# Performance work log

Hardware: AMD Instinct MI355X
Metric: run time of the kernel (lower is better)

The kernel has to match this reference:

```python
import jax, jax.numpy as jnp
import numpy as np

B, T, N, M = 128, 128, 32, 128  # batch, window(input_len), driving_series, hidden_size


def _lstm_cell(x_t, h, c, Wih, Whh, bih, bhh):
    # PyTorch gate order: i, f, g, o
    g = x_t @ Wih.T + bih + h @ Whh.T + bhh
    i, f, gg, o = jnp.split(g, 4, axis=-1)
    c = jax.nn.sigmoid(f) * c + jax.nn.sigmoid(i) * jnp.tanh(gg)
    h = jax.nn.sigmoid(o) * jnp.tanh(c)
    return h, c


def _lstm_seq(x, Wih, Whh, bih, bhh):
    # x: [B,T,n] -> outputs [B,T,m], zero init state
    Bc = x.shape[0]
    m = Whh.shape[1]
    def step(carry, x_t):
        h, c = carry
        h, c = _lstm_cell(x_t, h, c, Wih, Whh, bih, bhh)
        return (h, c), h
    h0 = jnp.zeros((Bc, m), x.dtype)
    (_, _), ys = jax.lax.scan(step, (h0, h0), jnp.swapaxes(x, 0, 1))
    return jnp.swapaxes(ys, 0, 1)


def _forward(x, Wih0, Whh0, bih0, bhh0, We, Ue, Ve,
             Wg, bg, Wa, ba,
             Wih1, Whh1, bih1, bhh1, Wih2, Whh2, bih2, bhh2):
    Bc, Tc, n = x.shape
    m = Whh0.shape[1]
    ux = jnp.einsum('btn,mn->btm', x, Ue)  # Ue(x), constant across steps

    def step(carry, x_t):
        h, c = carry
        hs = jnp.concatenate([h, c], axis=-1)              # [B,2m]
        e = jnp.tanh(ux + (hs @ We.T)[:, None, :]) @ Ve[0]  # [B,T]
        a = jax.nn.softmax(e, axis=1)
        ia_t = jnp.einsum('bt,btn->bn', a, x)              # attended input at step t
        h, c = _lstm_cell(x_t, h, c, Wih0, Whh0, bih0, bhh0)
        return (h, c), ia_t

    h0 = jnp.zeros((Bc, m), x.dtype)
    (_, _), ia = jax.lax.scan(step, (h0, h0), jnp.swapaxes(x, 0, 1))
    input_attention = jnp.swapaxes(ia, 0, 1)               # [B,T,n]

    # self (spatial) attention, fully vectorized over t
    g = jnp.tanh(jnp.einsum('btn,mn->btm', x, Wg) + bg)
    a = jax.nn.sigmoid(jnp.einsum('btm,nm->btn', g, Wa) + ba)
    self_attention = a * x                                  # [B,T,n]

    out1 = _lstm_seq(input_attention, Wih1, Whh1, bih1, bhh1)
    out2 = _lstm_seq(self_attention, Wih2, Whh2, bih2, bhh2)
    return jnp.concatenate([out1, out2], axis=-1)           # [B,T,2m]


def setup_inputs() -> dict:
    key = jax.random.key(0)
    ks = jax.random.split(key, 20)
    stdv = 1.0 / np.sqrt(M)
    u = lambda k, shp: jax.random.uniform(k, shp, jnp.float32, -stdv, stdv)
    inp = {
        'x': jax.random.normal(ks[0], (B, T, N), jnp.float32),
        'Wih0': u(ks[1], (4 * M, N)), 'Whh0': u(ks[2], (4 * M, M)),
        'bih0': u(ks[3], (4 * M,)), 'bhh0': u(ks[4], (4 * M,)),
        'We': u(ks[5], (M, 2 * M)), 'Ue': u(ks[6], (M, N)), 'Ve': u(ks[7], (1, M)),
        'Wg': u(ks[8], (M, N)), 'bg': u(ks[9], (M,)),
        'Wa': u(ks[10], (N, M)), 'ba': u(ks[11], (N,)),
        'Wih1': u(ks[12], (4 * M, N)), 'Whh1': u(ks[13], (4 * M, M)),
        'bih1': u(ks[14], (4 * M,)), 'bhh1': u(ks[15], (4 * M,)),
        'Wih2': u(ks[16], (4 * M, N)), 'Whh2': u(ks[17], (4 * M, M)),
        'bih2': u(ks[18], (4 * M,)), 'bhh2': u(ks[19], (4 * M,)),
    }
    return inp


def reference(x, Wih0, Whh0, bih0, bhh0, We, Ue, Ve, Wg, bg, Wa, ba,
              Wih1, Whh1, bih1, bhh1, Wih2, Whh2, bih2, bhh2):
    return _forward(x, Wih0, Whh0, bih0, bhh0, We, Ue, Ve, Wg, bg, Wa, ba,
                    Wih1, Whh1, bih1, bhh1, Wih2, Whh2, bih2, bhh2)
```

## Files before the change

### kernel.cpp

```cpp
#include <hip/hip_runtime.h>

#define DI __device__ __forceinline__

DI float frcp(float v)  { return __builtin_amdgcn_rcpf(v); }
DI float fsig(float v)  { return frcp(1.0f + __expf(-v)); }
DI float ftanh(float v) { return 1.0f - 2.0f * frcp(__expf(2.0f * v) + 1.0f); }
DI float dot4(float4 a, float4 b) { return a.x*b.x + a.y*b.y + a.z*b.z + a.w*b.w; }

DI unsigned bf16r(float f) {
    unsigned b = __float_as_uint(f);
    return (b + 0x7fffu + ((b >> 16) & 1u)) >> 16;
}
DI unsigned bfpack(float f0, float f1) { return bf16r(f0) | (bf16r(f1) << 16); }
DI float blo(unsigned u) { return __uint_as_float(u << 16); }
DI float bhi(unsigned u) { return __uint_as_float(u & 0xffff0000u); }

template <int MODE>
DI void lstm_scan3(const float* __restrict__ xin,
                   const float* __restrict__ Wih,
                   const float* __restrict__ Whh,
                   const float* __restrict__ bih,
                   const float* __restrict__ bhh,
                   float* __restrict__ rec,
                   float* __restrict__ outp,
                   float* lds)
{
    const int tid = threadIdx.x;
    const int r0 = tid & 127;
    const int kq = tid >> 7;
    float* xl = lds;
    float* hl = lds + 4096;
    float* pl = lds + 4224;

    for (int i = tid; i < 4096; i += 512) xl[i] = xin[i];
    if (tid < 128) hl[tid] = 0.f;

    unsigned wp[4][20];
    #pragma unroll
    for (int g = 0; g < 4; ++g) {
        const int r = g * 128 + r0;
        float4 wt[10];
        if (kq == 0) {
            const float4* pi4 = (const float4*)(Wih + r * 32);
            #pragma unroll
            for (int i = 0; i < 8; ++i) wt[i] = pi4[i];
            const float4* ph4 = (const float4*)(Whh + r * 128);
            wt[8] = ph4[0]; wt[9] = ph4[1];
        } else {
            const float4* ph4 = (const float4*)(Whh + r * 128 + 40 * kq - 32);
            #pragma unroll
            for (int i = 0; i < 10; ++i) wt[i] = ph4[i];
        }
        #pragma unroll
        for (int i = 0; i < 10; ++i) {
            wp[g][2*i]   = bfpack(wt[i].x, wt[i].y);
            wp[g][2*i+1] = bfpack(wt[i].z, wt[i].w);
        }
    }
    #pragma unroll
    for (int g = 0; g < 4; ++g)
        #pragma unroll
        for (int j = 0; j < 20; ++j)
            asm volatile("" : "+v"(wp[g][j]));

    float b0 = 0.f, b1 = 0.f, b2 = 0.f, b3 = 0.f, hreg = 0.f, creg = 0.f;
    if (tid < 128) {
        b0 = bih[tid]       + bhh[tid];
        b1 = bih[128 + tid] + bhh[128 + tid];
        b2 = bih[256 + tid] + bhh[256 + tid];
        b3 = bih[384 + tid] + bhh[384 + tid];
    }
    __syncthreads();

    for (int t = 0; t < 128; ++t) {
        float a[4] = {0.f, 0.f, 0.f, 0.f};
        if (kq == 0) {
            const float4* x4 = (const float4*)(xl + t * 32);
            #pragma unroll
            for (int j = 0; j < 8; ++j) {
                const float4 zj = x4[j];
                #pragma unroll
                for (int g = 0; g < 4; ++g) {
                    const unsigned u0 = wp[g][2*j], u1 = wp[g][2*j+1];
                    a[g] += blo(u0)*zj.x + bhi(u0)*zj.y + blo(u1)*zj.z + bhi(u1)*zj.w;
                }
            }
            const float4* h4 = (const float4*)hl;
            #pragma unroll
            for (int j = 8; j < 10; ++j) {
                const float4 zj = h4[j - 8];
                #pragma unroll
                for (int g = 0; g < 4; ++g) {
                    const unsigned u0 = wp[g][2*j], u1 = wp[g][2*j+1];
                    a[g] += blo(u0)*zj.x + bhi(u0)*zj.y + blo(u1)*zj.z + bhi(u1)*zj.w;
                }
            }
        } else {
            const float4* h4 = (const float4*)(hl + 40 * kq - 32);
            #pragma unroll
            for (int j = 0; j < 10; ++j) {
                const float4 zj = h4[j];
                #pragma unroll
                for (int g = 0; g < 4; ++g) {
                    const unsigned u0 = wp[g][2*j], u1 = wp[g][2*j+1];
                    a[g] += blo(u0)*zj.x + bhi(u0)*zj.y + blo(u1)*zj.z + bhi(u1)*zj.w;
                }
            }
        }
        pl[kq * 512 +       r0] = a[0];
        pl[kq * 512 + 128 + r0] = a[1];
        pl[kq * 512 + 256 + r0] = a[2];
        pl[kq * 512 + 384 + r0] = a[3];
        __syncthreads();
        if (tid < 128) {
            float pi = b0 + pl[tid]        + pl[512 + tid]  + pl[1024 + tid] + pl[1536 + tid];
            float pf = b1 + pl[128 + tid]  + pl[640 + tid]  + pl[1152 + tid] + pl[1664 + tid];
            float pg = b2 + pl[256 + tid]  + pl[768 + tid]  + pl[1280 + tid] + pl[1792 + tid];
            float po = b3 + pl[384 + tid]  + pl[896 + tid]  + pl[1408 + tid] + pl[1920 + tid];
            if (MODE == 0) {
                rec[t * 256 + tid]       = hreg;
                rec[t * 256 + 128 + tid] = creg;
            }
            float iv = fsig(pi), fv = fsig(pf), gv = ftanh(pg), ov = fsig(po);
            creg = fv * creg + iv * gv;
            hreg = ov * ftanh(creg);
            hl[tid] = hreg;
            if (MODE == 1) outp[t * 256 + tid] = hreg;
        }
        __syncthreads();
    }
}

DI void selfatt_body(const float* __restrict__ x, const float* __restrict__ Wg,
                     const float* __restrict__ bg, const float* __restrict__ Wa,
                     const float* __restrict__ ba, float* __restrict__ sa,
                     int b, float* s)
{
    float* xl  = s;
    float* Wgl = s + 4224;
    float* WaT = s + 8448;
    float* bgl = s + 12672;
    float* bal = s + 12800;
    float* gl  = s + 12832;
    float* pp  = s + 13344;

    const int tid = threadIdx.x;
    for (int i = tid; i < 4096; i += 512) {
        int r = i >> 5, n = i & 31;
        xl[r * 33 + n]  = x[b * 4096 + i];
        Wgl[r * 33 + n] = Wg[i];
        WaT[(i & 127) * 33 + (i >> 7)] = Wa[i];
    }
    if (tid < 128) bgl[tid] = bg[tid];
    else if (tid < 160) bal[tid - 128] = ba[tid - 128];
    __syncthreads();

    const int tl = tid >> 7;
    for (int it = 0; it < 32; ++it) {
        {   const int m = tid & 127;
            const int t = it * 4 + tl;
            float acc = bgl[m];
            #pragma unroll
            for (int n = 0; n < 32; ++n) acc += xl[t * 33 + n] * Wgl[m * 33 + n];
            gl[tl * 128 + m] = ftanh(acc);
        }
        __syncthreads();
        {   const int n = tid & 31, c = (tid >> 5) & 3;
            float acc = 0.f;
            #pragma unroll
            for (int j = 0; j < 32; ++j) {
                int m = c * 32 + j;
                acc += gl[tl * 128 + m] * WaT[m * 33 + n];
            }
            pp[(tl * 4 + c) * 32 + n] = acc;
        }
        __syncthreads();
        if (tid < 128) {
            const int tl2 = tid >> 5, n = tid & 31;
            const int t = it * 4 + tl2;
            float sv = pp[(tl2 * 4 + 0) * 32 + n] + pp[(tl2 * 4 + 1) * 32 + n]
                     + pp[(tl2 * 4 + 2) * 32 + n] + pp[(tl2 * 4 + 3) * 32 + n] + bal[n];
            sa[b * 4096 + t * 32 + n] = fsig(sv) * xl[t * 33 + n];
        }
        __syncthreads();
    }
}

__global__ __launch_bounds__(512)
void k1_lstm0_sa(const float* __restrict__ x,
                 const float* __restrict__ Wih0, const float* __restrict__ Whh0,
                 const float* __restrict__ bih0, const float* __restrict__ bhh0,
                 const float* __restrict__ Wg, const float* __restrict__ bg,
                 const float* __restrict__ Wa, const float* __restrict__ ba,
                 float* __restrict__ rec, float* __restrict__ sa)
{
    __shared__ float smem[13856];
    const int blk = blockIdx.x;
    if (blk < 128) {
        lstm_scan3<0>(x + blk * 4096, Wih0, Whh0, bih0, bhh0,
                      rec + blk * 32768, nullptr, smem);
    } else {
        selfatt_body(x, Wg, bg, Wa, ba, sa, blk - 128, smem);
    }
}

__global__ __launch_bounds__(512)
void k3_lstm12(const float* __restrict__ ia, const float* __restrict__ sa,
               const float* __restrict__ Wih1, const float* __restrict__ Whh1,
               const float* __restrict__ bih1, const float* __restrict__ bhh1,
               const float* __restrict__ Wih2, const float* __restrict__ Whh2,
               const float* __restrict__ bih2, const float* __restrict__ bhh2,
               float* __restrict__ out)
{
    __shared__ float smem[6272];
    const int blk = blockIdx.x;
    if (blk < 128) {
        lstm_scan3<1>(ia + blk * 4096, Wih1, Whh1, bih1, bhh1,
                      nullptr, out + blk * 32768, smem);
    } else {
        const int b = blk - 128;
        lstm_scan3<1>(sa + b * 4096, Wih2, Whh2, bih2, bhh2,
                      nullptr, out + b * 32768 + 128, smem);
    }
}

__global__ __launch_bounds__(512, 1)
void kP_w2(const float* __restrict__ We,
           float* __restrict__ rec)
{
    __shared__ float smem[12544];
    float* hsB  = smem;
    float* wbuf = smem + 8320;
    const int tid = threadIdx.x;
    const int b = blockIdx.x;
    const int m = tid >> 2, q = tid & 3;

    float4 wer[16];
    {
        const float4* p = (const float4*)(We + m * 256 + q * 64);
        #pragma unroll
        for (int i = 0; i < 16; ++i) wer[i] = p[i];
    }
    #pragma unroll
    for (int i = 0; i < 16; i += 4) {
        asm volatile("" : "+v"(wer[i].x), "+v"(wer[i].y), "+v"(wer[i].z), "+v"(wer[i].w),
                          "+v"(wer[i+1].x), "+v"(wer[i+1].y), "+v"(wer[i+1].z), "+v"(wer[i+1].w),
                          "+v"(wer[i+2].x), "+v"(wer[i+2].y), "+v"(wer[i+2].z), "+v"(wer[i+2].w),
                          "+v"(wer[i+3].x), "+v"(wer[i+3].y), "+v"(wer[i+3].z), "+v"(wer[i+3].w));
    }

    for (int tb = 0; tb < 4; ++tb) {
        __syncthreads();
        for (int i = tid; i < 8192; i += 512)
            hsB[(i >> 8) * 260 + (i & 255)] = rec[(long)b * 32768 + (tb * 32 + (i >> 8)) * 256 + (i & 255)];
        __syncthreads();
        for (int tl = 0; tl < 32; ++tl) {
            const float4* h4 = (const float4*)(hsB + tl * 260 + q * 64);
            float acc = 0.f;
            #pragma unroll
            for (int i = 0; i < 16; ++i) acc += dot4(wer[i], h4[i]);
            acc += __shfl_xor(acc, 1);
            acc += __shfl_xor(acc, 2);
            if (q == 0) wbuf[tl * 132 + m] = acc;
        }
        __syncthreads();
        for (int i = tid; i < 4096; i += 512)
            rec[(long)b * 32768 + tb * 4096 + i] = 2.0f * wbuf[(i >> 7) * 132 + (i & 127)];
    }
}

__global__ __launch_bounds__(512, 2)
void kB_attn(const float* __restrict__ x,
             const float* __restrict__ Ue,
             const float* __restrict__ Ve,
             const float* __restrict__ w2g,
             float* __restrict__ ia)
{
    __shared__ float xl[4608];
    __shared__ float wl[4224];
    __shared__ float uxc[4224];
    __shared__ float UeAv[4608];
    __shared__ float vel[128];
    __shared__ float sinv[32];
    __shared__ float iap[576];

    const int tid = threadIdx.x;
    const int b  = blockIdx.x >> 2;
    const int tc = blockIdx.x & 3;

    for (int i = tid; i < 4096; i += 512) {
        xl[(i >> 5) * 36 + (i & 31)]   = x[b * 4096 + i];
        UeAv[(i >> 5) * 36 + (i & 31)] = Ue[i];
        wl[(i >> 7) * 132 + (i & 127)] = w2g[(long)b * 32768 + (tc * 32 + (i >> 7)) * 128 + (i & 127)];
    }
    if (tid < 128) vel[tid] = 2.0f * Ve[tid];
    __syncthreads();

    const int ts = tid & 127, mg = tid >> 7;
    float4 xr[8];
    {
        const float4* xp = (const float4*)(xl + ts * 36);
        #pragma unroll
        for (int i = 0; i < 8; ++i) xr[i] = xp[i];
    }
    float VeTot = 0.f;
    for (int i = 0; i < 128; ++i) VeTot += vel[i];
    VeTot *= 0.5f;

    const int tp = tid >> 5, tg = tid & 31;
    const int t0 = 2 * tp, t1 = t0 + 1;
    float s0[4] = {0.f, 0.f, 0.f, 0.f};
    float s1[4] = {0.f, 0.f, 0.f, 0.f};

    for (int mc = 0; mc < 4; ++mc) {
        #pragma unroll
        for (int j = 0; j < 8; ++j) {
            const int ml = mg * 8 + j;
            const float4* u4 = (const float4*)(UeAv + (mc * 32 + ml) * 36);
            float acc = 0.f;
            #pragma unroll
            for (int i = 0; i < 8; ++i) acc += dot4(xr[i], u4[i]);
            uxc[ml * 132 + ts] = 2.0f * acc;
        }
        __syncthreads();
        #pragma unroll 8
        for (int ml = 0; ml < 32; ++ml) {
            const int m = mc * 32 + ml;
            const float vm = vel[m];
            const float w0 = wl[t0 * 132 + m];
            const float w1 = wl[t1 * 132 + m];
            const float4 u4 = *(const float4*)(uxc + ml * 132 + 4 * tg);
            s0[0] += vm * frcp(__expf(u4.x + w0) + 1.0f);
            s0[1] += vm * frcp(__expf(u4.y + w0) + 1.0f);
            s0[2] += vm * frcp(__expf(u4.z + w0) + 1.0f);
            s0[3] += vm * frcp(__expf(u4.w + w0) + 1.0f);
            s1[0] += vm * frcp(__expf(u4.x + w1) + 1.0f);
            s1[1] += vm * frcp(__expf(u4.y + w1) + 1.0f);
            s1[2] += vm * frcp(__expf(u4.z + w1) + 1.0f);
            s1[3] += vm * frcp(__expf(u4.w + w1) + 1.0f);
        }
        __syncthreads();
    }

    float e0[4], e1[4];
    #pragma unroll
    for (int j = 0; j < 4; ++j) { e0[j] = VeTot - s0[j]; e1[j] = VeTot - s1[j]; }
    float M0 = fmaxf(fmaxf(e0[0], e0[1]), fmaxf(e0[2], e0[3]));
    float M1 = fmaxf(fmaxf(e1[0], e1[1]), fmaxf(e1[2], e1[3]));
    #pragma unroll
    for (int o = 1; o < 32; o <<= 1) {
        M0 = fmaxf(M0, __shfl_xor(M0, o));
        M1 = fmaxf(M1, __shfl_xor(M1, o));
    }
    float a00 = __expf(e0[0] - M0), a01 = __expf(e0[1] - M0);
    float a02 = __expf(e0[2] - M0), a03 = __expf(e0[3] - M0);
    float a10 = __expf(e1[0] - M1), a11 = __expf(e1[1] - M1);
    float a12 = __expf(e1[2] - M1), a13 = __expf(e1[3] - M1);
    float S0 = a00 + a01 + a02 + a03;
    float S1 = a10 + a11 + a12 + a13;
    #pragma unroll
    for (int o = 1; o < 32; o <<= 1) {
        S0 += __shfl_xor(S0, o);
        S1 += __shfl_xor(S1, o);
    }
    float* av = UeAv;
    *(float4*)(av + t0 * 128 + 4 * tg) = make_float4(a00, a01, a02, a03);
    *(float4*)(av + t1 * 128 + 4 * tg) = make_float4(a10, a11, a12, a13);
    if (tg == 0) { sinv[t0] = frcp(S0); sinv[t1] = frcp(S1); }
    __syncthreads();

    const int gph = tid >> 5, n = tid & 31;
    for (int tl = 0; tl < 32; ++tl) {
        float acc = 0.f;
        #pragma unroll
        for (int j = 0; j < 8; ++j)
            acc += av[tl * 128 + gph * 8 + j] * xl[(gph * 8 + j) * 36 + n];
        iap[gph * 36 + n] = acc;
        __syncthreads();
        if (tid < 32) {
            float s = 0.f;
            #pragma unroll
            for (int g = 0; g < 16; ++g) s += iap[g * 36 + tid];
            ia[((long)(b * 128 + tc * 32 + tl)) * 32 + tid] = s * sinv[tl];
        }
        __syncthreads();
    }
}

extern "C" void kernel_launch(void* const* d_in, const int* in_sizes, int n_in,
                              void* d_out, int out_size, void* d_ws, size_t ws_size,
                              hipStream_t stream)
{
    const float* x    = (const float*)d_in[0];
    const float* Wih0 = (const float*)d_in[1];
    const float* Whh0 = (const float*)d_in[2];
    const float* bih0 = (const float*)d_in[3];
    const float* bhh0 = (const float*)d_in[4];
    const float* We   = (const float*)d_in[5];
    const float* Ue   = (const float*)d_in[6];
    const float* Ve   = (const float*)d_in[7];
    const float* Wg   = (const float*)d_in[8];
    const float* bg   = (const float*)d_in[9];
    const float* Wa   = (const float*)d_in[10];
    const float* ba   = (const float*)d_in[11];
    const float* Wih1 = (const float*)d_in[12];
    const float* Whh1 = (const float*)d_in[13];
    const float* bih1 = (const float*)d_in[14];
    const float* bhh1 = (const float*)d_in[15];
    const float* Wih2 = (const float*)d_in[16];
    const float* Whh2 = (const float*)d_in[17];
    const float* bih2 = (const float*)d_in[18];
    const float* bhh2 = (const float*)d_in[19];

    float* out = (float*)d_out;
    float* ws  = (float*)d_ws;
    float* sa  = ws;
    float* rec = ws + 524288;
    float* iaw = ws + 4718592;

    k1_lstm0_sa<<<256, 512, 0, stream>>>(x, Wih0, Whh0, bih0, bhh0,
                                         Wg, bg, Wa, ba, rec, sa);
    kP_w2<<<128, 512, 0, stream>>>(We, rec);
    kB_attn<<<512, 512, 0, stream>>>(x, Ue, Ve, rec, iaw);
    k3_lstm12<<<256, 512, 0, stream>>>(iaw, sa, Wih1, Whh1, bih1, bhh1,
                                       Wih2, Whh2, bih2, bhh2, out);
}
```

Measured before the change: 537.9 us.

## Use packed fp16 dot2 for LSTM recurrence and split W2 projection across blocks

After: 454.1 us. 15.6% less time.

```diff
diff --git a/kernel.cpp b/kernel.cpp
--- a/kernel.cpp
+++ b/kernel.cpp
@@ -1,22 +1,29 @@
 #include <hip/hip_runtime.h>
 
 #define DI __device__ __forceinline__
+
+typedef _Float16 h2v __attribute__((ext_vector_type(2)));
 
 DI float frcp(float v)  { return __builtin_amdgcn_rcpf(v); }
 DI float fsig(float v)  { return frcp(1.0f + __expf(-v)); }
 DI float ftanh(float v) { return 1.0f - 2.0f * frcp(__expf(2.0f * v) + 1.0f); }
 DI float dot4(float4 a, float4 b) { return a.x*b.x + a.y*b.y + a.z*b.z + a.w*b.w; }
 
-DI unsigned bf16r(float f) {
-    unsigned b = __float_as_uint(f);
-    return (b + 0x7fffu + ((b >> 16) & 1u)) >> 16;
-}
-DI unsigned bfpack(float f0, float f1) { return bf16r(f0) | (bf16r(f1) << 16); }
-DI float blo(unsigned u) { return __uint_as_float(u << 16); }
-DI float bhi(unsigned u) { return __uint_as_float(u & 0xffff0000u); }
+DI h2v      u2h(unsigned u) { return __builtin_bit_cast(h2v, u); }
+DI unsigned pkrtz(float a, float b) {
+    return __builtin_bit_cast(unsigned, __builtin_amdgcn_cvt_pkrtz(a, b));
+}
+
+DI float fdot2w(h2v a, h2v b, float c) {
+#if __has_builtin(__builtin_amdgcn_fdot2)
+    return __builtin_amdgcn_fdot2(a, b, c, false);
+#else
+    return c + (float)a.x * (float)b.x + (float)a.y * (float)b.y;
+#endif
+}
 
 template <int MODE>
-DI void lstm_scan3(const float* __restrict__ xin,
+DI void lstm_scan4(const float* __restrict__ xin,
                    const float* __restrict__ Wih,
                    const float* __restrict__ Whh,
                    const float* __restrict__ bih,
@@ -28,14 +35,17 @@
     const int tid = threadIdx.x;
     const int r0 = tid & 127;
     const int kq = tid >> 7;
-    float* xl = lds;
-    float* hl = lds + 4096;
-    float* pl = lds + 4224;
-
-    for (int i = tid; i < 4096; i += 512) xl[i] = xin[i];
-    if (tid < 128) hl[tid] = 0.f;
-
-    unsigned wp[4][20];
+    unsigned* xp = (unsigned*)lds;
+    unsigned* hp = (unsigned*)lds + 2048;
+    float* pl = lds + 2112;
+
+    for (int i = tid; i < 2048; i += 512) {
+        const float2 v = *(const float2*)(xin + 2 * i);
+        xp[i] = pkrtz(v.x, v.y);
+    }
+    if (tid < 64) hp[tid] = 0u;
+
+    unsigned wpu[4][20];
     #pragma unroll
     for (int g = 0; g < 4; ++g) {
         const int r = g * 128 + r0;
@@ -53,80 +63,71 @@
         }
         #pragma unroll
         for (int i = 0; i < 10; ++i) {
-            wp[g][2*i]   = bfpack(wt[i].x, wt[i].y);
-            wp[g][2*i+1] = bfpack(wt[i].z, wt[i].w);
+            wpu[g][2*i]   = pkrtz(wt[i].x, wt[i].y);
+            wpu[g][2*i+1] = pkrtz(wt[i].z, wt[i].w);
         }
     }
     #pragma unroll
     for (int g = 0; g < 4; ++g)
         #pragma unroll
         for (int j = 0; j < 20; ++j)
-            asm volatile("" : "+v"(wp[g][j]));
-
-    float b0 = 0.f, b1 = 0.f, b2 = 0.f, b3 = 0.f, hreg = 0.f, creg = 0.f;
-    if (tid < 128) {
-        b0 = bih[tid]       + bhh[tid];
-        b1 = bih[128 + tid] + bhh[128 + tid];
-        b2 = bih[256 + tid] + bhh[256 + tid];
-        b3 = bih[384 + tid] + bhh[384 + tid];
-    }
+            asm volatile("" : "+v"(wpu[g][j]));
+
+    const int rr = tid >> 2;
+    const int gg = tid & 3;
+    const float bias = bih[gg * 128 + rr] + bhh[gg * 128 + rr];
+    const float nl_a = (gg == 2) ? 2.0f : 1.0f;
+    const float nl_b = (gg == 2) ? -1.0f : 0.0f;
+    float hreg = 0.f, creg = 0.f;
     __syncthreads();
 
     for (int t = 0; t < 128; ++t) {
-        float a[4] = {0.f, 0.f, 0.f, 0.f};
+        uint4 z0, z1, z2, z3, ze;
         if (kq == 0) {
-            const float4* x4 = (const float4*)(xl + t * 32);
-            #pragma unroll
-            for (int j = 0; j < 8; ++j) {
-                const float4 zj = x4[j];
-                #pragma unroll
-                for (int g = 0; g < 4; ++g) {
-                    const unsigned u0 = wp[g][2*j], u1 = wp[g][2*j+1];
-                    a[g] += blo(u0)*zj.x + bhi(u0)*zj.y + blo(u1)*zj.z + bhi(u1)*zj.w;
-                }
+            const uint4* x4 = (const uint4*)(xp + t * 16);
+            z0 = x4[0]; z1 = x4[1]; z2 = x4[2]; z3 = x4[3];
+            ze = *(const uint4*)hp;
+        } else {
+            const uint4* h4 = (const uint4*)(hp + 20 * kq - 16);
+            z0 = h4[0]; z1 = h4[1]; z2 = h4[2]; z3 = h4[3]; ze = h4[4];
+        }
+        float a0 = 0.f, a1 = 0.f, a2 = 0.f, a3 = 0.f;
+        #define DG(J, U) { const h2v zz = u2h(U); \
+            a0 = fdot2w(u2h(wpu[0][J]), zz, a0); \
+            a1 = fdot2w(u2h(wpu[1][J]), zz, a1); \
+            a2 = fdot2w(u2h(wpu[2][J]), zz, a2); \
+            a3 = fdot2w(u2h(wpu[3][J]), zz, a3); }
+        DG(0,  z0.x) DG(1,  z0.y) DG(2,  z0.z) DG(3,  z0.w)
+        DG(4,  z1.x) DG(5,  z1.y) DG(6,  z1.z) DG(7,  z1.w)
+        DG(8,  z2.x) DG(9,  z2.y) DG(10, z2.z) DG(11, z2.w)
+        DG(12, z3.x) DG(13, z3.y) DG(14, z3.z) DG(15, z3.w)
+        DG(16, ze.x) DG(17, ze.y) DG(18, ze.z) DG(19, ze.w)
+        #undef DG
+        pl[kq * 544 +       r0] = a0;
+        pl[kq * 544 + 136 + r0] = a1;
+        pl[kq * 544 + 272 + r0] = a2;
+        pl[kq * 544 + 408 + r0] = a3;
+        __syncthreads();
+
+        float s = bias + pl[gg * 136 + rr]        + pl[544 + gg * 136 + rr]
+                       + pl[1088 + gg * 136 + rr] + pl[1632 + gg * 136 + rr];
+        float sg  = frcp(1.0f + __expf(-(nl_a * s)));
+        float val = nl_a * sg + nl_b;
+        float v1 = __shfl_xor(val, 1);
+        float v2 = __shfl_xor(val, 2);
+        float v3 = __shfl_xor(val, 3);
+        float cn = v1 * creg + val * v2;
+        float hn = v3 * ftanh(cn);
+        float hn_hi = __shfl_down(hn, 4);
+        if (gg == 0) {
+            if (MODE == 0) {
+                rec[t * 256 + rr]       = hreg;
+                rec[t * 256 + 128 + rr] = creg;
             }
-            const float4* h4 = (const float4*)hl;
-            #pragma unroll
-            for (int j = 8; j < 10; ++j) {
-                const float4 zj = h4[j - 8];
-                #pragma unroll
-                for (int g = 0; g < 4; ++g) {
-                    const unsigned u0 = wp[g][2*j], u1 = wp[g][2*j+1];
-                    a[g] += blo(u0)*zj.x + bhi(u0)*zj.y + blo(u1)*zj.z + bhi(u1)*zj.w;
-                }
-            }
-        } else {
-            const float4* h4 = (const float4*)(hl + 40 * kq - 32);
-            #pragma unroll
-            for (int j = 0; j < 10; ++j) {
-                const float4 zj = h4[j];
-                #pragma unroll
-                for (int g = 0; g < 4; ++g) {
-                    const unsigned u0 = wp[g][2*j], u1 = wp[g][2*j+1];
-                    a[g] += blo(u0)*zj.x + bhi(u0)*zj.y + blo(u1)*zj.z + bhi(u1)*zj.w;
-                }
-            }
-        }
-        pl[kq * 512 +       r0] = a[0];
-        pl[kq * 512 + 128 + r0] = a[1];
-        pl[kq * 512 + 256 + r0] = a[2];
-        pl[kq * 512 + 384 + r0] = a[3];
-        __syncthreads();
-        if (tid < 128) {
-            float pi = b0 + pl[tid]        + pl[512 + tid]  + pl[1024 + tid] + pl[1536 + tid];
-            float pf = b1 + pl[128 + tid]  + pl[640 + tid]  + pl[1152 + tid] + pl[1664 + tid];
-            float pg = b2 + pl[256 + tid]  + pl[768 + tid]  + pl[1280 + tid] + pl[1792 + tid];
-            float po = b3 + pl[384 + tid]  + pl[896 + tid]  + pl[1408 + tid] + pl[1920 + tid];
-            if (MODE == 0) {
-                rec[t * 256 + tid]       = hreg;
-                rec[t * 256 + 128 + tid] = creg;
-            }
-            float iv = fsig(pi), fv = fsig(pf), gv = ftanh(pg), ov = fsig(po);
-            creg = fv * creg + iv * gv;
-            hreg = ov * ftanh(creg);
-            hl[tid] = hreg;
-            if (MODE == 1) outp[t * 256 + tid] = hreg;
-        }
+            creg = cn; hreg = hn;
+            if (MODE == 1) outp[t * 256 + rr] = hn;
+        }
+        if ((tid & 7) == 0) hp[rr >> 1] = pkrtz(hn, hn_hi);
         __syncthreads();
     }
 }
@@ -197,7 +198,7 @@
     __shared__ float smem[13856];
     const int blk = blockIdx.x;
     if (blk < 128) {
-        lstm_scan3<0>(x + blk * 4096, Wih0, Whh0, bih0, bhh0,
+        lstm_scan4<0>(x + blk * 4096, Wih0, Whh0, bih0, bhh0,
                       rec + blk * 32768, nullptr, smem);
     } else {
         selfatt_body(x, Wg, bg, Wa, ba, sa, blk - 128, smem);
@@ -212,21 +213,67 @@
                const float* __restrict__ bih2, const float* __restrict__ bhh2,
                float* __restrict__ out)
 {
-    __shared__ float smem[6272];
+    __shared__ float smem[4288];
     const int blk = blockIdx.x;
     if (blk < 128) {
-        lstm_scan3<1>(ia + blk * 4096, Wih1, Whh1, bih1, bhh1,
+        lstm_scan4<1>(ia + blk * 4096, Wih1, Whh1, bih1, bhh1,
                       nullptr, out + blk * 32768, smem);
     } else {
         const int b = blk - 128;
-        lstm_scan3<1>(sa + b * 4096, Wih2, Whh2, bih2, bhh2,
+        lstm_scan4<1>(sa + b * 4096, Wih2, Whh2, bih2, bhh2,
                       nullptr, out + b * 32768 + 128, smem);
     }
 }
 
 __global__ __launch_bounds__(512, 1)
-void kP_w2(const float* __restrict__ We,
-           float* __restrict__ rec)
+void kP_w2_sep(const float* __restrict__ We, const float* __restrict__ rec,
+               float* __restrict__ w2)
+{
+    __shared__ float smem[12544];
+    float* hsB  = smem;
+    float* wbuf = smem + 8320;
+    const int tid = threadIdx.x;
+    const int b  = blockIdx.x >> 1;
+    const int hh = blockIdx.x & 1;
+    const int m = tid >> 2, q = tid & 3;
+
+    float4 wer[16];
+    {
+        const float4* p = (const float4*)(We + m * 256 + q * 64);
+        #pragma unroll
+        for (int i = 0; i < 16; ++i) wer[i] = p[i];
+    }
+    #pragma unroll
+    for (int i = 0; i < 16; i += 4) {
+        asm volatile("" : "+v"(wer[i].x), "+v"(wer[i].y), "+v"(wer[i].z), "+v"(wer[i].w),
+                          "+v"(wer[i+1].x), "+v"(wer[i+1].y), "+v"(wer[i+1].z), "+v"(wer[i+1].w),
+                          "+v"(wer[i+2].x), "+v"(wer[i+2].y), "+v"(wer[i+2].z), "+v"(wer[i+2].w),
+                          "+v"(wer[i+3].x), "+v"(wer[i+3].y), "+v"(wer[i+3].z), "+v"(wer[i+3].w));
+    }
+
+    for (int t2 = 0; t2 < 2; ++t2) {
+        const int tb = hh * 2 + t2;
+        __syncthreads();
+        for (int i = tid; i < 8192; i += 512)
+            hsB[(i >> 8) * 260 + (i & 255)] = rec[(long)b * 32768 + (tb * 32 + (i >> 8)) * 256 + (i & 255)];
+        __syncthreads();
+        for (int tl = 0; tl < 32; ++tl) {
+            const float4* h4 = (const float4*)(hsB + tl * 260 + q * 64);
+            float acc = 0.f;
+            #pragma unroll
+            for (int i = 0; i < 16; ++i) acc += dot4(wer[i], h4[i]);
+            acc += __shfl_xor(acc, 1);
+            acc += __shfl_xor(acc, 2);
+            if (q == 0) wbuf[tl * 132 + m] = acc;
+        }
+        __syncthreads();
+        for (int i = tid; i < 4096; i += 512)
+            w2[(long)b * 16384 + tb * 4096 + i] = 2.0f * wbuf[(i >> 7) * 132 + (i & 127)];
+    }
+}
+
+__global__ __launch_bounds__(512, 1)
+void kP_w2_inplace(const float* __restrict__ We, float* __restrict__ rec)
 {
     __shared__ float smem[12544];
     float* hsB  = smem;
@@ -274,6 +321,7 @@
              const float* __restrict__ Ue,
              const float* __restrict__ Ve,
              const float* __restrict__ w2g,
+             long bstr,
              float* __restrict__ ia)
 {
     __shared__ float xl[4608];
@@ -291,7 +339,7 @@
     for (int i = tid; i < 4096; i += 512) {
         xl[(i >> 5) * 36 + (i & 31)]   = x[b * 4096 + i];
         UeAv[(i >> 5) * 36 + (i & 31)] = Ue[i];
-        wl[(i >> 7) * 132 + (i & 127)] = w2g[(long)b * 32768 + (tc * 32 + (i >> 7)) * 128 + (i & 127)];
+        wl[(i >> 7) * 132 + (i & 127)] = w2g[(long)b * bstr + (tc * 32 + (i >> 7)) * 128 + (i & 127)];
     }
     if (tid < 128) vel[tid] = 2.0f * Ve[tid];
     __syncthreads();
@@ -417,11 +465,18 @@
     float* sa  = ws;
     float* rec = ws + 524288;
     float* iaw = ws + 4718592;
+    float* w2  = ws + 5242880;
+    const bool sep = ws_size >= (size_t)7340032 * 4;
 
     k1_lstm0_sa<<<256, 512, 0, stream>>>(x, Wih0, Whh0, bih0, bhh0,
                                          Wg, bg, Wa, ba, rec, sa);
-    kP_w2<<<128, 512, 0, stream>>>(We, rec);
-    kB_attn<<<512, 512, 0, stream>>>(x, Ue, Ve, rec, iaw);
+    if (sep) {
+        kP_w2_sep<<<256, 512, 0, stream>>>(We, rec, w2);
+        kB_attn<<<512, 512, 0, stream>>>(x, Ue, Ve, w2, 16384L, iaw);
+    } else {
+        kP_w2_inplace<<<128, 512, 0, stream>>>(We, rec);
+        kB_attn<<<512, 512, 0, stream>>>(x, Ue, Ve, rec, 32768L, iaw);
+    }
     k3_lstm12<<<256, 512, 0, stream>>>(iaw, sa, Wih1, Whh1, bih1, bhh1,
                                        Wih2, Whh2, bih2, bhh2, out);
 }
```
